# Kernel optimization log

Hardware: AMD Instinct MI355X
Metric: run time of the kernel (lower is better)

The kernel has to match this reference:

```python
import jax, jax.numpy as jnp
import numpy as np

N, E, D, H = 50000, 800000, 128, 8
DH = D // H  # 16
EPS_LN = 1e-5


def layer_norm(x, gamma, beta):
    mu = jnp.mean(x, axis=-1, keepdims=True)
    var = jnp.var(x, axis=-1, keepdims=True)
    return (x - mu) * jax.lax.rsqrt(var + EPS_LN) * gamma + beta


def setup_inputs() -> dict:
    key = jax.random.key(0)
    ks = jax.random.split(key, 12)
    s = 1.0 / np.sqrt(D)
    x = jax.random.normal(ks[0], (N, D), dtype=jnp.float32)
    src = jax.random.randint(ks[1], (E,), 0, N, dtype=jnp.int32)
    dst = jax.random.randint(ks[2], (E,), 0, N, dtype=jnp.int32)
    Wq = jax.random.normal(ks[3], (D, D), dtype=jnp.float32) * s
    Wk = jax.random.normal(ks[4], (D, D), dtype=jnp.float32) * s
    Wv = jax.random.normal(ks[5], (D, D), dtype=jnp.float32) * s
    Wo = jax.random.normal(ks[6], (D, D), dtype=jnp.float32) * s
    bq = jnp.zeros((D,), jnp.float32)
    bk = jnp.zeros((D,), jnp.float32)
    bv = jnp.zeros((D,), jnp.float32)
    bo = jnp.zeros((D,), jnp.float32)
    gamma1 = jnp.ones((D,), jnp.float32)
    beta1 = jnp.zeros((D,), jnp.float32)
    gamma2 = jnp.ones((D,), jnp.float32)
    beta2 = jnp.zeros((D,), jnp.float32)
    return dict(x=x, src=src, dst=dst, Wq=Wq, bq=bq, Wk=Wk, bk=bk, Wv=Wv, bv=bv,
                Wo=Wo, bo=bo, gamma1=gamma1, beta1=beta1, gamma2=gamma2, beta2=beta2)


def reference(x, src, dst, Wq, bq, Wk, bk, Wv, bv, Wo, bo, gamma1, beta1, gamma2, beta2):
    n = x.shape[0]
    Q = (x @ Wq + bq).reshape(n, H, DH)   # [N,H,Dh]
    K = (x @ Wk + bk).reshape(n, H, DH)
    V = (x @ Wv + bv).reshape(n, H, DH)
    # edge-wise QK dot: score[e,h] = sum_d K[src[e],h,d] * Q[dst[e],h,d]
    score = jnp.sum(K[src] * Q[dst], axis=-1) / np.sqrt(DH)  # [E,H]
    score = jnp.exp(jnp.clip(score, -5.0, 5.0))
    # scatter-sum weighted values and normalizer over destination nodes
    wV = jax.ops.segment_sum(V[src] * score[..., None], dst, num_segments=n)  # [N,H,Dh]
    z = jax.ops.segment_sum(score, dst, num_segments=n)                        # [N,H]
    attn = (wV / (z[..., None] + 1e-3)).reshape(n, D)
    h = layer_norm(x + attn, gamma1, beta1)
    # sublayer: h + relu(O(LN(h)))  (dropout = 0)
    h = h + jax.nn.relu(layer_norm(h, gamma2, beta2) @ Wo + bo)
    return h
```

## Files before the change

### kernel.cpp

```cpp
#include <hip/hip_runtime.h>
#include <hip/hip_bf16.h>

typedef unsigned short ushort_t;
typedef __attribute__((ext_vector_type(8))) short short8;
typedef __attribute__((ext_vector_type(4))) float floatx4;

__device__ __forceinline__ unsigned short f2bf(float f) {
    union { float f; unsigned u; } x; x.f = f;
    unsigned r = x.u + 0x7fffu + ((x.u >> 16) & 1u);
    return (unsigned short)(r >> 16);
}
__device__ __forceinline__ float bf2f(unsigned short u) {
    union { unsigned u; float f; } x; x.u = ((unsigned)u) << 16; return x.f;
}
__device__ __forceinline__ float u2f(unsigned u) {
    union { unsigned u; float f; } x; x.u = u; return x.f;
}

__global__ __launch_bounds__(256) void transpose_swz(
    const float* __restrict__ Wq, const float* __restrict__ Wk,
    const float* __restrict__ Wv, const float* __restrict__ Wo,
    ushort_t* __restrict__ out)
{
    const float* W = (blockIdx.y == 0) ? Wq : (blockIdx.y == 1) ? Wk :
                     (blockIdx.y == 2) ? Wv : Wo;
    ushort_t* T = out + (size_t)blockIdx.y * 128 * 128;
    int t = blockIdx.x * 256 + threadIdx.x;
    int kg = t >> 7;
    int n  = t & 127;
    int k0 = kg * 8;
    short8 v;
    #pragma unroll
    for (int j = 0; j < 8; j++)
        v[j] = (short)f2bf(W[(size_t)(k0 + j) * 128 + n]);
    int sn = n >> 4, l15 = n & 15, kb = kg >> 2, quad = kg & 3;
    size_t f = ((size_t)((sn * 4 + kb) * 4 + quad)) * 128 + (size_t)l15 * 8;
    *(short8*)(T + f) = v;
}

__global__ __launch_bounds__(256) void gemm_qkv(
    const float* __restrict__ X, const ushort_t* __restrict__ Wsw,
    const float* __restrict__ bq, const float* __restrict__ bk, const float* __restrict__ bv,
    ushort_t* __restrict__ Q, ushort_t* __restrict__ KV, int M,
    const int* __restrict__ dst, int* __restrict__ deg, int E)
{
    __shared__ ushort_t Xs[64 * 136];
    int tid = threadIdx.x;
    int rowBase = blockIdx.x * 64;
    int wsel = blockIdx.y;
    const ushort_t* Wmat = Wsw + (size_t)wsel * 128 * 128;
    const float* bias = (wsel == 0) ? bq : (wsel == 1) ? bk : bv;

    {
        int nblk = gridDim.x * gridDim.y;
        int fb = blockIdx.y * gridDim.x + blockIdx.x;
        int per = (E + nblk - 1) / nblk;
        int end = min(per * (fb + 1), E);
        for (int i = per * fb + tid; i < end; i += 256)
            atomicAdd(&deg[dst[i]], 1);
    }

    int r = tid >> 4;
    int c = (tid & 15) * 8;
    for (int rr = 0; rr < 64; rr += 16) {
        int row = rowBase + rr + r;
        int rc = (row < M) ? row : (M - 1);
        const float* p = X + (size_t)rc * 128 + c;
        float4 f0 = *(const float4*)p;
        float4 f1 = *(const float4*)(p + 4);
        short8 v;
        v[0] = (short)f2bf(f0.x); v[1] = (short)f2bf(f0.y);
        v[2] = (short)f2bf(f0.z); v[3] = (short)f2bf(f0.w);
        v[4] = (short)f2bf(f1.x); v[5] = (short)f2bf(f1.y);
        v[6] = (short)f2bf(f1.z); v[7] = (short)f2bf(f1.w);
        *(short8*)&Xs[(rr + r) * 136 + c] = v;
    }
    __syncthreads();

    int lane = tid & 63, wave = tid >> 6;
    int wm = wave * 16;
    int l15 = lane & 15, quad = lane >> 4;
    floatx4 acc[8] = {};
    for (int kb = 0; kb < 4; kb++) {
        short8 a = *(const short8*)&Xs[(wm + l15) * 136 + kb * 32 + quad * 8];
        for (int sn = 0; sn < 8; sn++) {
            short8 b = *(const short8*)(Wmat + (size_t)(sn * 4 + kb) * 512 + lane * 8);
            acc[sn] = __builtin_amdgcn_mfma_f32_16x16x32_bf16(a, b, acc[sn], 0, 0, 0);
        }
    }

    for (int sn = 0; sn < 8; sn++) {
        int col = sn * 16 + l15;
        float bia = bias[col];
        for (int rr2 = 0; rr2 < 4; rr2++) {
            int rl = wm + quad * 4 + rr2;
            Xs[rl * 136 + col] = f2bf(acc[sn][rr2] + bia);
        }
    }
    for (int it = 0; it < 4; it++) {
        int idx = it * 64 + lane;
        int rl = idx >> 4;
        int seg = idx & 15;
        int row = rowBase + wm + rl;
        if (row < M) {
            short8 v = *(const short8*)&Xs[(wm + rl) * 136 + seg * 8];
            if (wsel == 0) {
                *(short8*)(Q + (size_t)row * 128 + seg * 8) = v;
            } else {
                *(short8*)(KV + (size_t)row * 256 + seg * 16 + ((wsel == 2) ? 8 : 0)) = v;
            }
        }
    }
}

__global__ __launch_bounds__(256) void k_scan_blocks(const int* __restrict__ deg, int* __restrict__ offs,
                                                     int* __restrict__ bsums, int n) {
    __shared__ int s[256];
    int i = blockIdx.x * 256 + threadIdx.x;
    int v = (i < n) ? deg[i] : 0;
    s[threadIdx.x] = v;
    __syncthreads();
    for (int d = 1; d < 256; d <<= 1) {
        int t = (threadIdx.x >= d) ? s[threadIdx.x - d] : 0;
        __syncthreads();
        s[threadIdx.x] += t;
        __syncthreads();
    }
    int incl = s[threadIdx.x];
    if (i < n) offs[i] = incl - v;
    if (threadIdx.x == 255) bsums[blockIdx.x] = incl;
}

__global__ __launch_bounds__(256) void k_add_base(int* __restrict__ offs, int* __restrict__ cursor,
                                                  const int* __restrict__ bs, int nb, int n, int E) {
    int tid = threadIdx.x;
    int acc = 0;
    for (int t = tid; t < nb; t += 256)
        if (t < (int)blockIdx.x) acc += bs[t];
    for (int m = 1; m < 64; m <<= 1) acc += __shfl_xor(acc, m, 64);
    __shared__ int sw[4];
    if ((tid & 63) == 0) sw[tid >> 6] = acc;
    __syncthreads();
    int base = sw[0] + sw[1] + sw[2] + sw[3];
    int i = blockIdx.x * 256 + tid;
    if (i < n) {
        int o = offs[i] + base;
        offs[i] = o;
        cursor[i] = o;
    }
    if (blockIdx.x == 0 && tid == 0) offs[n] = E;
}

__global__ __launch_bounds__(256) void k_scatter(const int* __restrict__ src, const int* __restrict__ dst,
                                                 int* __restrict__ cursor, int* __restrict__ eadj, int E) {
    int i = blockIdx.x * 256 + threadIdx.x;
    if (i < E) {
        int p = atomicAdd(&cursor[dst[i]], 1);
        eadj[p] = src[i];
    }
}

__global__ __launch_bounds__(256) void edge_attn(
    const ushort_t* __restrict__ Qb, const ushort_t* __restrict__ KV,
    const float* __restrict__ xin,
    const int* __restrict__ offs, const int* __restrict__ eadj,
    const float* __restrict__ g1, const float* __restrict__ be1,
    const float* __restrict__ g2, const float* __restrict__ be2,
    ushort_t* __restrict__ h1out, ushort_t* __restrict__ ln2out, int N)
{
    int wave = threadIdx.x >> 6, lane = threadIdx.x & 63;
    int n = blockIdx.x * 4 + wave;
    if (n >= N) return;
    int l15 = lane & 15, grp = lane >> 4;

    uint4 qp = *(const uint4*)(Qb + (size_t)n * 128 + l15 * 8);
    float q0 = u2f(qp.x << 16), q1 = u2f(qp.x & 0xffff0000u);
    float q2 = u2f(qp.y << 16), q3 = u2f(qp.y & 0xffff0000u);
    float q4 = u2f(qp.z << 16), q5 = u2f(qp.z & 0xffff0000u);
    float q6 = u2f(qp.w << 16), q7 = u2f(qp.w & 0xffff0000u);

    int s0 = offs[n], s1 = offs[n + 1];
    float a0=0.f,a1=0.f,a2=0.f,a3=0.f,a4=0.f,a5=0.f,a6=0.f,a7=0.f,z=0.f;
    for (int base = s0; base < s1; base += 64) {
        int cnt = min(s1 - base, 64);
        int ee = (base + lane < s1) ? eadj[base + lane] : 0;
        #pragma unroll 2
        for (int j = 0; j < cnt; j += 4) {
            int jj = j + grp;
            int sn = __shfl(ee, jj, 64);
            const ushort_t* kvp = KV + (size_t)sn * 256 + l15 * 16;
            uint4 kk = *(const uint4*)kvp;
            uint4 vv = *(const uint4*)(kvp + 8);
            float d0 = fmaf(q1, u2f(kk.x & 0xffff0000u), q0 * u2f(kk.x << 16));
            float d1 = fmaf(q3, u2f(kk.y & 0xffff0000u), q2 * u2f(kk.y << 16));
            float d2 = fmaf(q5, u2f(kk.z & 0xffff0000u), q4 * u2f(kk.z << 16));
            float d3 = fmaf(q7, u2f(kk.w & 0xffff0000u), q6 * u2f(kk.w << 16));
            float d = (d0 + d1) + (d2 + d3);
            d += __shfl_xor(d, 1, 64);
            float sc = fminf(5.f, fmaxf(-5.f, d * 0.25f));
            float e = (jj < cnt) ? __expf(sc) : 0.f;
            a0 = fmaf(e, u2f(vv.x << 16), a0); a1 = fmaf(e, u2f(vv.x & 0xffff0000u), a1);
            a2 = fmaf(e, u2f(vv.y << 16), a2); a3 = fmaf(e, u2f(vv.y & 0xffff0000u), a3);
            a4 = fmaf(e, u2f(vv.z << 16), a4); a5 = fmaf(e, u2f(vv.z & 0xffff0000u), a5);
            a6 = fmaf(e, u2f(vv.w << 16), a6); a7 = fmaf(e, u2f(vv.w & 0xffff0000u), a7);
            z += e;
        }
    }
    a0 += __shfl_xor(a0, 16, 64); a0 += __shfl_xor(a0, 32, 64);
    a1 += __shfl_xor(a1, 16, 64); a1 += __shfl_xor(a1, 32, 64);
    a2 += __shfl_xor(a2, 16, 64); a2 += __shfl_xor(a2, 32, 64);
    a3 += __shfl_xor(a3, 16, 64); a3 += __shfl_xor(a3, 32, 64);
    a4 += __shfl_xor(a4, 16, 64); a4 += __shfl_xor(a4, 32, 64);
    a5 += __shfl_xor(a5, 16, 64); a5 += __shfl_xor(a5, 32, 64);
    a6 += __shfl_xor(a6, 16, 64); a6 += __shfl_xor(a6, 32, 64);
    a7 += __shfl_xor(a7, 16, 64); a7 += __shfl_xor(a7, 32, 64);
    z  += __shfl_xor(z, 16, 64);  z  += __shfl_xor(z, 32, 64);
    float inv = 1.f / (z + 1e-3f);

    const float* xr = xin + (size_t)n * 128 + l15 * 8;
    float4 xa = *(const float4*)xr;
    float4 xb = *(const float4*)(xr + 4);
    float t0 = xa.x + a0 * inv, t1 = xa.y + a1 * inv;
    float t2 = xa.z + a2 * inv, t3 = xa.w + a3 * inv;
    float t4 = xb.x + a4 * inv, t5 = xb.y + a5 * inv;
    float t6 = xb.z + a6 * inv, t7 = xb.w + a7 * inv;

    float s  = t0 + t1 + t2 + t3 + t4 + t5 + t6 + t7;
    float s2 = t0*t0 + t1*t1 + t2*t2 + t3*t3 + t4*t4 + t5*t5 + t6*t6 + t7*t7;
    for (int m = 1; m < 16; m <<= 1) { s += __shfl_xor(s, m, 64); s2 += __shfl_xor(s2, m, 64); }
    float mu = s * (1.f / 128.f);
    float var = s2 * (1.f / 128.f) - mu * mu;
    float rstd = rsqrtf(var + 1e-5f);

    const float* g1r = g1 + l15 * 8;
    const float* b1r = be1 + l15 * 8;
    float4 ga = *(const float4*)g1r, gb = *(const float4*)(g1r + 4);
    float4 ba = *(const float4*)b1r, bb = *(const float4*)(b1r + 4);
    float h0 = (t0 - mu) * rstd * ga.x + ba.x;
    float h1 = (t1 - mu) * rstd * ga.y + ba.y;
    float h2 = (t2 - mu) * rstd * ga.z + ba.z;
    float h3 = (t3 - mu) * rstd * ga.w + ba.w;
    float h4 = (t4 - mu) * rstd * gb.x + bb.x;
    float h5 = (t5 - mu) * rstd * gb.y + bb.y;
    float h6 = (t6 - mu) * rstd * gb.z + bb.z;
    float h7 = (t7 - mu) * rstd * gb.w + bb.w;
    if (grp == 0) {
        uint4 pk;
        pk.x = (unsigned)f2bf(h0) | ((unsigned)f2bf(h1) << 16);
        pk.y = (unsigned)f2bf(h2) | ((unsigned)f2bf(h3) << 16);
        pk.z = (unsigned)f2bf(h4) | ((unsigned)f2bf(h5) << 16);
        pk.w = (unsigned)f2bf(h6) | ((unsigned)f2bf(h7) << 16);
        *(uint4*)(h1out + (size_t)n * 128 + l15 * 8) = pk;
    }

    s  = h0 + h1 + h2 + h3 + h4 + h5 + h6 + h7;
    s2 = h0*h0 + h1*h1 + h2*h2 + h3*h3 + h4*h4 + h5*h5 + h6*h6 + h7*h7;
    for (int m = 1; m < 16; m <<= 1) { s += __shfl_xor(s, m, 64); s2 += __shfl_xor(s2, m, 64); }
    float mu2 = s * (1.f / 128.f);
    float var2 = s2 * (1.f / 128.f) - mu2 * mu2;
    float rstd2 = rsqrtf(var2 + 1e-5f);

    const float* g2r = g2 + l15 * 8;
    const float* b2r = be2 + l15 * 8;
    float4 gc = *(const float4*)g2r, gd = *(const float4*)(g2r + 4);
    float4 bc = *(const float4*)b2r, bd = *(const float4*)(b2r + 4);
    float l0 = (h0 - mu2) * rstd2 * gc.x + bc.x;
    float l1 = (h1 - mu2) * rstd2 * gc.y + bc.y;
    float l2 = (h2 - mu2) * rstd2 * gc.z + bc.z;
    float l3 = (h3 - mu2) * rstd2 * gc.w + bc.w;
    float l4 = (h4 - mu2) * rstd2 * gd.x + bd.x;
    float l5 = (h5 - mu2) * rstd2 * gd.y + bd.y;
    float l6 = (h6 - mu2) * rstd2 * gd.z + bd.z;
    float l7 = (h7 - mu2) * rstd2 * gd.w + bd.w;
    if (grp == 1) {
        uint4 pk;
        pk.x = (unsigned)f2bf(l0) | ((unsigned)f2bf(l1) << 16);
        pk.y = (unsigned)f2bf(l2) | ((unsigned)f2bf(l3) << 16);
        pk.z = (unsigned)f2bf(l4) | ((unsigned)f2bf(l5) << 16);
        pk.w = (unsigned)f2bf(l6) | ((unsigned)f2bf(l7) << 16);
        *(uint4*)(ln2out + (size_t)n * 128 + l15 * 8) = pk;
    }
}

__global__ __launch_bounds__(256) void gemm_o(
    const ushort_t* __restrict__ X, const ushort_t* __restrict__ Wsw,
    const float* __restrict__ bo, const ushort_t* __restrict__ h1in,
    float* __restrict__ Out, int M)
{
    __shared__ ushort_t As[64 * 136];
    int tid = threadIdx.x;
    int rowBase = blockIdx.x * 64;
    int snBase = blockIdx.y * 4;
    int colBase = snBase * 16;

    int r = tid >> 4;
    int c = (tid & 15) * 8;
    for (int rr = 0; rr < 64; rr += 16) {
        int row = rowBase + rr + r;
        int rc = (row < M) ? row : (M - 1);
        short8 v = *(const short8*)(X + (size_t)rc * 128 + c);
        *(short8*)&As[(rr + r) * 136 + c] = v;
    }
    __syncthreads();

    int lane = tid & 63, wave = tid >> 6;
    int wm = wave * 16;
    int l15 = lane & 15, quad = lane >> 4;
    floatx4 acc[4] = {};
    for (int kb = 0; kb < 4; kb++) {
        short8 a = *(const short8*)&As[(wm + l15) * 136 + kb * 32 + quad * 8];
        for (int s = 0; s < 4; s++) {
            short8 b = *(const short8*)(Wsw + (size_t)((snBase + s) * 4 + kb) * 512 + lane * 8);
            acc[s] = __builtin_amdgcn_mfma_f32_16x16x32_bf16(a, b, acc[s], 0, 0, 0);
        }
    }

    float* Cs = (float*)As;
    for (int s = 0; s < 4; s++) {
        int cl = s * 16 + l15;
        float bia = bo[colBase + cl];
        for (int rr2 = 0; rr2 < 4; rr2++) {
            int rl = wm + quad * 4 + rr2;
            Cs[rl * 68 + cl] = fmaxf(acc[s][rr2] + bia, 0.f);
        }
    }
    for (int it = 0; it < 4; it++) {
        int idx = it * 64 + lane;
        int rl = idx >> 4;
        int c4 = (idx & 15) * 4;
        int row = rowBase + wm + rl;
        if (row < M) {
            float4 v = *(const float4*)&Cs[(wm + rl) * 68 + c4];
            uint2 hp = *(const uint2*)(h1in + (size_t)row * 128 + colBase + c4);
            v.x += u2f(hp.x << 16);
            v.y += u2f(hp.x & 0xffff0000u);
            v.z += u2f(hp.y << 16);
            v.w += u2f(hp.y & 0xffff0000u);
            *(float4*)(Out + (size_t)row * 128 + colBase + c4) = v;
        }
    }
}

extern "C" void kernel_launch(void* const* d_in, const int* in_sizes, int n_in,
                              void* d_out, int out_size, void* d_ws, size_t ws_size,
                              hipStream_t stream) {
    const int D = 128;
    const int N = in_sizes[0] / D;
    const int E = in_sizes[1];

    const float* x   = (const float*)d_in[0];
    const int*   src = (const int*)d_in[1];
    const int*   dst = (const int*)d_in[2];
    const float* Wq  = (const float*)d_in[3];
    const float* bq  = (const float*)d_in[4];
    const float* Wk  = (const float*)d_in[5];
    const float* bk  = (const float*)d_in[6];
    const float* Wv  = (const float*)d_in[7];
    const float* bv  = (const float*)d_in[8];
    const float* Wo  = (const float*)d_in[9];
    const float* bo  = (const float*)d_in[10];
    const float* g1  = (const float*)d_in[11];
    const float* be1 = (const float*)d_in[12];
    const float* g2  = (const float*)d_in[13];
    const float* be2 = (const float*)d_in[14];

    char* ws = (char*)d_ws;
    size_t o = 0;
    auto alloc = [&](size_t b) { o = (o + 255) & ~(size_t)255; size_t r = o; o += b; return r; };
    ushort_t* Qb   = (ushort_t*)(ws + alloc((size_t)N * D * 2));
    ushort_t* KVb  = (ushort_t*)(ws + alloc((size_t)N * D * 4));
    ushort_t* ln2  = (ushort_t*)(ws + alloc((size_t)N * D * 2));
    ushort_t* h1   = (ushort_t*)(ws + alloc((size_t)N * D * 2));
    ushort_t* Wt   = (ushort_t*)(ws + alloc((size_t)4 * 128 * 128 * 2));
    int*      deg  = (int*)(ws + alloc((size_t)N * 4));
    int*      offs = (int*)(ws + alloc((size_t)(N + 1) * 4));
    int*      cur  = (int*)(ws + alloc((size_t)N * 4));
    int*      bsum = (int*)(ws + alloc((size_t)256 * 4));
    int*      eadj = (int*)(ws + alloc((size_t)E * 4));

    int nScanBlocks = (N + 255) / 256;
    int nEdgeBlocks = (E + 255) / 256;
    int nRowTiles = (N + 63) / 64;

    hipMemsetAsync(deg, 0, (size_t)N * 4, stream);
    transpose_swz<<<dim3(8, 4), 256, 0, stream>>>(Wq, Wk, Wv, Wo, Wt);
    gemm_qkv<<<dim3(nRowTiles, 3), 256, 0, stream>>>(x, Wt, bq, bk, bv, Qb, KVb, N, dst, deg, E);
    k_scan_blocks<<<nScanBlocks, 256, 0, stream>>>(deg, offs, bsum, N);
    k_add_base<<<nScanBlocks, 256, 0, stream>>>(offs, cur, bsum, nScanBlocks, N, E);
    k_scatter<<<nEdgeBlocks, 256, 0, stream>>>(src, dst, cur, eadj, E);
    edge_attn<<<(N + 3) / 4, 256, 0, stream>>>(Qb, KVb, x, offs, eadj, g1, be1, g2, be2, h1, ln2, N);
    gemm_o<<<dim3(nRowTiles, 2), 256, 0, stream>>>(ln2, Wt + 3 * 128 * 128, bo, h1, (float*)d_out, N);
}
```

Measured before the change: 271.8 us.

## Switch intermediates from bf16 to fp16 with packed-half edge math and exp2

Changes all intermediates (Q, K, V, h1, LN2 output, weights) from bf16 to fp16, using the f16 MFMA and packed cvt_pkrtz conversions. The edge loop now uses fdot2 for the QK dot product, packed half FMA for the V accumulation, and exp2 with the log2(e)/4 scale folded into Q. The LayerNorm epilogue is redistributed so each lane handles 2 columns instead of 8, removing redundant per-group computation. The deg memset is folded into the transpose kernel, saving one launch. The risks are fp16 range and precision loss in the V accumulation and the cross-lane half reductions.

```diff
diff --git a/kernel.cpp b/kernel.cpp
--- a/kernel.cpp
+++ b/kernel.cpp
@@ -1,27 +1,47 @@
 #include <hip/hip_runtime.h>
-#include <hip/hip_bf16.h>
 
 typedef unsigned short ushort_t;
 typedef __attribute__((ext_vector_type(8))) short short8;
 typedef __attribute__((ext_vector_type(4))) float floatx4;
-
-__device__ __forceinline__ unsigned short f2bf(float f) {
-    union { float f; unsigned u; } x; x.f = f;
-    unsigned r = x.u + 0x7fffu + ((x.u >> 16) & 1u);
-    return (unsigned short)(r >> 16);
-}
-__device__ __forceinline__ float bf2f(unsigned short u) {
-    union { unsigned u; float f; } x; x.u = ((unsigned)u) << 16; return x.f;
-}
-__device__ __forceinline__ float u2f(unsigned u) {
-    union { unsigned u; float f; } x; x.u = u; return x.f;
+typedef __attribute__((ext_vector_type(2))) _Float16 half2v;
+typedef __attribute__((ext_vector_type(8))) _Float16 half8;
+
+#define QSCALE 0.36067376022224085f
+#define SCLIP  7.2134752044448170f
+
+__device__ __forceinline__ unsigned h2u(half2v h) {
+    union { half2v h; unsigned u; } x; x.h = h; return x.u;
+}
+__device__ __forceinline__ half2v u2h(unsigned u) {
+    union { unsigned u; half2v h; } x; x.u = u; return x.h;
+}
+__device__ __forceinline__ ushort_t h2us(_Float16 h) {
+    union { _Float16 h; ushort_t u; } x; x.h = h; return x.u;
+}
+__device__ __forceinline__ unsigned pkrtz(float a, float b) {
+    auto h = __builtin_amdgcn_cvt_pkrtz(a, b);
+    union { decltype(h) h2; unsigned u; } x; x.h2 = h; return x.u;
+}
+__device__ __forceinline__ float dot2h(half2v a, half2v b, float c) {
+#if __has_builtin(__builtin_amdgcn_fdot2)
+    return __builtin_amdgcn_fdot2(a, b, c, false);
+#else
+    return c + (float)a[0] * (float)b[0] + (float)a[1] * (float)b[1];
+#endif
+}
+__device__ __forceinline__ half2v pk_shfl_add(half2v a, int m) {
+    unsigned o = (unsigned)__shfl_xor((int)h2u(a), m, 64);
+    return a + u2h(o);
 }
 
 __global__ __launch_bounds__(256) void transpose_swz(
     const float* __restrict__ Wq, const float* __restrict__ Wk,
     const float* __restrict__ Wv, const float* __restrict__ Wo,
-    ushort_t* __restrict__ out)
+    ushort_t* __restrict__ out, int* __restrict__ deg, int N)
 {
+    int flat = (blockIdx.y * gridDim.x + blockIdx.x) * 256 + threadIdx.x;
+    for (int i = flat; i < N; i += 8192) deg[i] = 0;
+
     const float* W = (blockIdx.y == 0) ? Wq : (blockIdx.y == 1) ? Wk :
                      (blockIdx.y == 2) ? Wv : Wo;
     ushort_t* T = out + (size_t)blockIdx.y * 128 * 128;
@@ -29,13 +49,18 @@
     int kg = t >> 7;
     int n  = t & 127;
     int k0 = kg * 8;
-    short8 v;
+    float w[8];
     #pragma unroll
     for (int j = 0; j < 8; j++)
-        v[j] = (short)f2bf(W[(size_t)(k0 + j) * 128 + n]);
+        w[j] = W[(size_t)(k0 + j) * 128 + n];
+    int4 o;
+    o.x = (int)pkrtz(w[0], w[1]);
+    o.y = (int)pkrtz(w[2], w[3]);
+    o.z = (int)pkrtz(w[4], w[5]);
+    o.w = (int)pkrtz(w[6], w[7]);
     int sn = n >> 4, l15 = n & 15, kb = kg >> 2, quad = kg & 3;
     size_t f = ((size_t)((sn * 4 + kb) * 4 + quad)) * 128 + (size_t)l15 * 8;
-    *(short8*)(T + f) = v;
+    *(int4*)(T + f) = o;
 }
 
 __global__ __launch_bounds__(256) void gemm_qkv(
@@ -68,12 +93,12 @@
         const float* p = X + (size_t)rc * 128 + c;
         float4 f0 = *(const float4*)p;
         float4 f1 = *(const float4*)(p + 4);
-        short8 v;
-        v[0] = (short)f2bf(f0.x); v[1] = (short)f2bf(f0.y);
-        v[2] = (short)f2bf(f0.z); v[3] = (short)f2bf(f0.w);
-        v[4] = (short)f2bf(f1.x); v[5] = (short)f2bf(f1.y);
-        v[6] = (short)f2bf(f1.z); v[7] = (short)f2bf(f1.w);
-        *(short8*)&Xs[(rr + r) * 136 + c] = v;
+        int4 pv;
+        pv.x = (int)pkrtz(f0.x, f0.y);
+        pv.y = (int)pkrtz(f0.z, f0.w);
+        pv.z = (int)pkrtz(f1.x, f1.y);
+        pv.w = (int)pkrtz(f1.z, f1.w);
+        *(int4*)&Xs[(rr + r) * 136 + c] = pv;
     }
     __syncthreads();
 
@@ -82,19 +107,20 @@
     int l15 = lane & 15, quad = lane >> 4;
     floatx4 acc[8] = {};
     for (int kb = 0; kb < 4; kb++) {
-        short8 a = *(const short8*)&Xs[(wm + l15) * 136 + kb * 32 + quad * 8];
+        half8 a = *(const half8*)&Xs[(wm + l15) * 136 + kb * 32 + quad * 8];
         for (int sn = 0; sn < 8; sn++) {
-            short8 b = *(const short8*)(Wmat + (size_t)(sn * 4 + kb) * 512 + lane * 8);
-            acc[sn] = __builtin_amdgcn_mfma_f32_16x16x32_bf16(a, b, acc[sn], 0, 0, 0);
-        }
-    }
-
+            half8 b = *(const half8*)(Wmat + (size_t)(sn * 4 + kb) * 512 + lane * 8);
+            acc[sn] = __builtin_amdgcn_mfma_f32_16x16x32_f16(a, b, acc[sn], 0, 0, 0);
+        }
+    }
+
+    float scl = (wsel == 0) ? QSCALE : 1.0f;
     for (int sn = 0; sn < 8; sn++) {
         int col = sn * 16 + l15;
         float bia = bias[col];
         for (int rr2 = 0; rr2 < 4; rr2++) {
             int rl = wm + quad * 4 + rr2;
-            Xs[rl * 136 + col] = f2bf(acc[sn][rr2] + bia);
+            Xs[rl * 136 + col] = h2us((_Float16)((acc[sn][rr2] + bia) * scl));
         }
     }
     for (int it = 0; it < 4; it++) {
@@ -174,13 +200,11 @@
     int l15 = lane & 15, grp = lane >> 4;
 
     uint4 qp = *(const uint4*)(Qb + (size_t)n * 128 + l15 * 8);
-    float q0 = u2f(qp.x << 16), q1 = u2f(qp.x & 0xffff0000u);
-    float q2 = u2f(qp.y << 16), q3 = u2f(qp.y & 0xffff0000u);
-    float q4 = u2f(qp.z << 16), q5 = u2f(qp.z & 0xffff0000u);
-    float q6 = u2f(qp.w << 16), q7 = u2f(qp.w & 0xffff0000u);
+    half2v q0 = u2h(qp.x), q1 = u2h(qp.y), q2 = u2h(qp.z), q3 = u2h(qp.w);
 
     int s0 = offs[n], s1 = offs[n + 1];
-    float a0=0.f,a1=0.f,a2=0.f,a3=0.f,a4=0.f,a5=0.f,a6=0.f,a7=0.f,z=0.f;
+    half2v a01 = u2h(0u), a23 = u2h(0u), a45 = u2h(0u), a67 = u2h(0u);
+    float z = 0.f;
     for (int base = s0; base < s1; base += 64) {
         int cnt = min(s1 - base, 64);
         int ee = (base + lane < s1) ? eadj[base + lane] : 0;
@@ -191,95 +215,62 @@
             const ushort_t* kvp = KV + (size_t)sn * 256 + l15 * 16;
             uint4 kk = *(const uint4*)kvp;
             uint4 vv = *(const uint4*)(kvp + 8);
-            float d0 = fmaf(q1, u2f(kk.x & 0xffff0000u), q0 * u2f(kk.x << 16));
-            float d1 = fmaf(q3, u2f(kk.y & 0xffff0000u), q2 * u2f(kk.y << 16));
-            float d2 = fmaf(q5, u2f(kk.z & 0xffff0000u), q4 * u2f(kk.z << 16));
-            float d3 = fmaf(q7, u2f(kk.w & 0xffff0000u), q6 * u2f(kk.w << 16));
-            float d = (d0 + d1) + (d2 + d3);
+            float d = dot2h(u2h(kk.x), q0,
+                      dot2h(u2h(kk.y), q1,
+                      dot2h(u2h(kk.z), q2,
+                      dot2h(u2h(kk.w), q3, 0.f))));
             d += __shfl_xor(d, 1, 64);
-            float sc = fminf(5.f, fmaxf(-5.f, d * 0.25f));
-            float e = (jj < cnt) ? __expf(sc) : 0.f;
-            a0 = fmaf(e, u2f(vv.x << 16), a0); a1 = fmaf(e, u2f(vv.x & 0xffff0000u), a1);
-            a2 = fmaf(e, u2f(vv.y << 16), a2); a3 = fmaf(e, u2f(vv.y & 0xffff0000u), a3);
-            a4 = fmaf(e, u2f(vv.z << 16), a4); a5 = fmaf(e, u2f(vv.z & 0xffff0000u), a5);
-            a6 = fmaf(e, u2f(vv.w << 16), a6); a7 = fmaf(e, u2f(vv.w & 0xffff0000u), a7);
+            float sc = fminf(SCLIP, fmaxf(-SCLIP, d));
+            float e = (jj < cnt) ? exp2f(sc) : 0.f;
+            _Float16 eh = (_Float16)e;
+            half2v ep; ep[0] = eh; ep[1] = eh;
+            a01 += u2h(vv.x) * ep;
+            a23 += u2h(vv.y) * ep;
+            a45 += u2h(vv.z) * ep;
+            a67 += u2h(vv.w) * ep;
             z += e;
         }
     }
-    a0 += __shfl_xor(a0, 16, 64); a0 += __shfl_xor(a0, 32, 64);
-    a1 += __shfl_xor(a1, 16, 64); a1 += __shfl_xor(a1, 32, 64);
-    a2 += __shfl_xor(a2, 16, 64); a2 += __shfl_xor(a2, 32, 64);
-    a3 += __shfl_xor(a3, 16, 64); a3 += __shfl_xor(a3, 32, 64);
-    a4 += __shfl_xor(a4, 16, 64); a4 += __shfl_xor(a4, 32, 64);
-    a5 += __shfl_xor(a5, 16, 64); a5 += __shfl_xor(a5, 32, 64);
-    a6 += __shfl_xor(a6, 16, 64); a6 += __shfl_xor(a6, 32, 64);
-    a7 += __shfl_xor(a7, 16, 64); a7 += __shfl_xor(a7, 32, 64);
-    z  += __shfl_xor(z, 16, 64);  z  += __shfl_xor(z, 32, 64);
+    a01 = pk_shfl_add(a01, 16); a01 = pk_shfl_add(a01, 32);
+    a23 = pk_shfl_add(a23, 16); a23 = pk_shfl_add(a23, 32);
+    a45 = pk_shfl_add(a45, 16); a45 = pk_shfl_add(a45, 32);
+    a67 = pk_shfl_add(a67, 16); a67 = pk_shfl_add(a67, 32);
+    z += __shfl_xor(z, 16, 64); z += __shfl_xor(z, 32, 64);
     float inv = 1.f / (z + 1e-3f);
 
-    const float* xr = xin + (size_t)n * 128 + l15 * 8;
-    float4 xa = *(const float4*)xr;
-    float4 xb = *(const float4*)(xr + 4);
-    float t0 = xa.x + a0 * inv, t1 = xa.y + a1 * inv;
-    float t2 = xa.z + a2 * inv, t3 = xa.w + a3 * inv;
-    float t4 = xb.x + a4 * inv, t5 = xb.y + a5 * inv;
-    float t6 = xb.z + a6 * inv, t7 = xb.w + a7 * inv;
-
-    float s  = t0 + t1 + t2 + t3 + t4 + t5 + t6 + t7;
-    float s2 = t0*t0 + t1*t1 + t2*t2 + t3*t3 + t4*t4 + t5*t5 + t6*t6 + t7*t7;
-    for (int m = 1; m < 16; m <<= 1) { s += __shfl_xor(s, m, 64); s2 += __shfl_xor(s2, m, 64); }
+    half2v ap = (grp == 0) ? a01 : (grp == 1) ? a23 : (grp == 2) ? a45 : a67;
+    int col = l15 * 8 + grp * 2;
+    float a0 = (float)ap[0], a1 = (float)ap[1];
+
+    float2 xv = *(const float2*)(xin + (size_t)n * 128 + col);
+    float t0 = fmaf(a0, inv, xv.x);
+    float t1 = fmaf(a1, inv, xv.y);
+
+    float s = t0 + t1, s2 = t0 * t0 + t1 * t1;
+    #pragma unroll
+    for (int m = 1; m < 64; m <<= 1) { s += __shfl_xor(s, m, 64); s2 += __shfl_xor(s2, m, 64); }
     float mu = s * (1.f / 128.f);
     float var = s2 * (1.f / 128.f) - mu * mu;
     float rstd = rsqrtf(var + 1e-5f);
 
-    const float* g1r = g1 + l15 * 8;
-    const float* b1r = be1 + l15 * 8;
-    float4 ga = *(const float4*)g1r, gb = *(const float4*)(g1r + 4);
-    float4 ba = *(const float4*)b1r, bb = *(const float4*)(b1r + 4);
-    float h0 = (t0 - mu) * rstd * ga.x + ba.x;
-    float h1 = (t1 - mu) * rstd * ga.y + ba.y;
-    float h2 = (t2 - mu) * rstd * ga.z + ba.z;
-    float h3 = (t3 - mu) * rstd * ga.w + ba.w;
-    float h4 = (t4 - mu) * rstd * gb.x + bb.x;
-    float h5 = (t5 - mu) * rstd * gb.y + bb.y;
-    float h6 = (t6 - mu) * rstd * gb.z + bb.z;
-    float h7 = (t7 - mu) * rstd * gb.w + bb.w;
-    if (grp == 0) {
-        uint4 pk;
-        pk.x = (unsigned)f2bf(h0) | ((unsigned)f2bf(h1) << 16);
-        pk.y = (unsigned)f2bf(h2) | ((unsigned)f2bf(h3) << 16);
-        pk.z = (unsigned)f2bf(h4) | ((unsigned)f2bf(h5) << 16);
-        pk.w = (unsigned)f2bf(h6) | ((unsigned)f2bf(h7) << 16);
-        *(uint4*)(h1out + (size_t)n * 128 + l15 * 8) = pk;
-    }
-
-    s  = h0 + h1 + h2 + h3 + h4 + h5 + h6 + h7;
-    s2 = h0*h0 + h1*h1 + h2*h2 + h3*h3 + h4*h4 + h5*h5 + h6*h6 + h7*h7;
-    for (int m = 1; m < 16; m <<= 1) { s += __shfl_xor(s, m, 64); s2 += __shfl_xor(s2, m, 64); }
+    float2 gv = *(const float2*)(g1 + col);
+    float2 bv = *(const float2*)(be1 + col);
+    float h0 = (t0 - mu) * rstd * gv.x + bv.x;
+    float h1 = (t1 - mu) * rstd * gv.y + bv.y;
+    *(unsigned*)(h1out + (size_t)n * 128 + col) = pkrtz(h0, h1);
+
+    s = h0 + h1; s2 = h0 * h0 + h1 * h1;
+    #pragma unroll
+    for (int m = 1; m < 64; m <<= 1) { s += __shfl_xor(s, m, 64); s2 += __shfl_xor(s2, m, 64); }
     float mu2 = s * (1.f / 128.f);
     float var2 = s2 * (1.f / 128.f) - mu2 * mu2;
     float rstd2 = rsqrtf(var2 + 1e-5f);
 
-    const float* g2r = g2 + l15 * 8;
-    const float* b2r = be2 + l15 * 8;
-    float4 gc = *(const float4*)g2r, gd = *(const float4*)(g2r + 4);
-    float4 bc = *(const float4*)b2r, bd = *(const float4*)(b2r + 4);
-    float l0 = (h0 - mu2) * rstd2 * gc.x + bc.x;
-    float l1 = (h1 - mu2) * rstd2 * gc.y + bc.y;
-    float l2 = (h2 - mu2) * rstd2 * gc.z + bc.z;
-    float l3 = (h3 - mu2) * rstd2 * gc.w + bc.w;
-    float l4 = (h4 - mu2) * rstd2 * gd.x + bd.x;
-    float l5 = (h5 - mu2) * rstd2 * gd.y + bd.y;
-    float l6 = (h6 - mu2) * rstd2 * gd.z + bd.z;
-    float l7 = (h7 - mu2) * rstd2 * gd.w + bd.w;
-    if (grp == 1) {
-        uint4 pk;
-        pk.x = (unsigned)f2bf(l0) | ((unsigned)f2bf(l1) << 16);
-        pk.y = (unsigned)f2bf(l2) | ((unsigned)f2bf(l3) << 16);
-        pk.z = (unsigned)f2bf(l4) | ((unsigned)f2bf(l5) << 16);
-        pk.w = (unsigned)f2bf(l6) | ((unsigned)f2bf(l7) << 16);
-        *(uint4*)(ln2out + (size_t)n * 128 + l15 * 8) = pk;
-    }
+    float2 g2v = *(const float2*)(g2 + col);
+    float2 b2v = *(const float2*)(be2 + col);
+    float l0 = (h0 - mu2) * rstd2 * g2v.x + b2v.x;
+    float l1 = (h1 - mu2) * rstd2 * g2v.y + b2v.y;
+    *(unsigned*)(ln2out + (size_t)n * 128 + col) = pkrtz(l0, l1);
 }
 
 __global__ __launch_bounds__(256) void gemm_o(
@@ -308,10 +299,10 @@
     int l15 = lane & 15, quad = lane >> 4;
     floatx4 acc[4] = {};
     for (int kb = 0; kb < 4; kb++) {
-        short8 a = *(const short8*)&As[(wm + l15) * 136 + kb * 32 + quad * 8];
+        half8 a = *(const half8*)&As[(wm + l15) * 136 + kb * 32 + quad * 8];
         for (int s = 0; s < 4; s++) {
-            short8 b = *(const short8*)(Wsw + (size_t)((snBase + s) * 4 + kb) * 512 + lane * 8);
-            acc[s] = __builtin_amdgcn_mfma_f32_16x16x32_bf16(a, b, acc[s], 0, 0, 0);
+            half8 b = *(const half8*)(Wsw + (size_t)((snBase + s) * 4 + kb) * 512 + lane * 8);
+            acc[s] = __builtin_amdgcn_mfma_f32_16x16x32_f16(a, b, acc[s], 0, 0, 0);
         }
     }
 
@@ -332,10 +323,11 @@
         if (row < M) {
             float4 v = *(const float4*)&Cs[(wm + rl) * 68 + c4];
             uint2 hp = *(const uint2*)(h1in + (size_t)row * 128 + colBase + c4);
-            v.x += u2f(hp.x << 16);
-            v.y += u2f(hp.x & 0xffff0000u);
-            v.z += u2f(hp.y << 16);
-            v.w += u2f(hp.y & 0xffff0000u);
+            half2v ha = u2h(hp.x), hb = u2h(hp.y);
+            v.x += (float)ha[0];
+            v.y += (float)ha[1];
+            v.z += (float)hb[0];
+            v.w += (float)hb[1];
             *(float4*)(Out + (size_t)row * 128 + colBase + c4) = v;
         }
     }
@@ -382,8 +374,7 @@
     int nEdgeBlocks = (E + 255) / 256;
     int nRowTiles = (N + 63) / 64;
 
-    hipMemsetAsync(deg, 0, (size_t)N * 4, stream);
-    transpose_swz<<<dim3(8, 4), 256, 0, stream>>>(Wq, Wk, Wv, Wo, Wt);
+    transpose_swz<<<dim3(8, 4), 256, 0, stream>>>(Wq, Wk, Wv, Wo, Wt, deg, N);
     gemm_qkv<<<dim3(nRowTiles, 3), 256, 0, stream>>>(x, Wt, bq, bk, bv, Qb, KVb, N, dst, deg, E);
     k_scan_blocks<<<nScanBlocks, 256, 0, stream>>>(deg, offs, bsum, N);
     k_add_base<<<nScanBlocks, 256, 0, stream>>>(offs, cur, bsum, nScanBlocks, N, E);
```

Result: no change. 267.7 us (-1.5%).
